# Optimization experiments

Hardware: AMD Instinct MI355X
Metric: run time of the kernel (lower is better)

Reference implementation:

```python
import jax, jax.numpy as jnp
import numpy as np

D_MODEL = 2048
D_FFN = 8192
TOP_K = 256


def setup_inputs() -> dict:
    key = jax.random.key(0)
    kx, kg, ku, kd = jax.random.split(key, 4)
    B, S = 4, 2048
    x = jax.random.normal(kx, (B, S, D_MODEL), dtype=jnp.float32)
    # kaiming_uniform_(a=sqrt(5)) on a 2D tensor -> U(-1/sqrt(fan_in), 1/sqrt(fan_in)),
    # where PyTorch's fan_in is size(1) of the parameter.
    bg = 1.0 / np.sqrt(D_FFN)
    w_gate = jax.random.uniform(kg, (D_MODEL, D_FFN), jnp.float32, -bg, bg)
    w_up = jax.random.uniform(ku, (D_MODEL, D_FFN), jnp.float32, -bg, bg)
    bd = 1.0 / np.sqrt(D_MODEL)
    w_down = jax.random.uniform(kd, (D_FFN, D_MODEL), jnp.float32, -bd, bd)
    return {"x": x, "w_gate": w_gate, "w_up": w_up, "w_down": w_down}


def reference(x, w_gate, w_up, w_down):
    orig_shape = x.shape
    xf = x.reshape(-1, x.shape[-1])          # [N, d_model]
    G = xf @ w_gate                           # [N, d_ffn]
    U = xf @ w_up                             # [N, d_ffn]
    _, idx = jax.lax.top_k(G, TOP_K)          # [N, k] int32 indices into d_ffn
    Gk = jnp.take_along_axis(G, idx, axis=-1)  # [N, k]
    Uk = jnp.take_along_axis(U, idx, axis=-1)  # [N, k]
    Z = jax.nn.silu(Gk) * Uk                   # fused sparse SiLU activation, [N, k]
    # Sparse-to-dense down projection: scatter the k active channels per token
    # back into d_ffn (top-k indices are unique per row, so .set is exact),
    # then a single dense matmul with w_down.
    N = G.shape[0]
    Zd = jnp.zeros((N, D_FFN), dtype=Z.dtype).at[jnp.arange(N)[:, None], idx].set(Z)
    out = Zd @ w_down                          # [N, d_model]
    return out.reshape(*orig_shape[:-1], w_down.shape[-1])
```

## Files before the change

kernel.cpp:

```cpp
#include <hip/hip_runtime.h>
#include <hip/hip_bf16.h>
#include <stdint.h>

#define D_MODEL 2048
#define D_FFN   8192
#define NTOK    8192
#define TOPK    256

typedef __bf16 bf16x8 __attribute__((ext_vector_type(8)));
typedef __bf16 bf16x4 __attribute__((ext_vector_type(4)));
typedef float  f32x4  __attribute__((ext_vector_type(4)));

__device__ inline void load_lds16(const void* g, void* l) {
    __builtin_amdgcn_global_load_lds((__attribute__((address_space(1))) void*)g,
                                     (__attribute__((address_space(3))) void*)l,
                                     16, 0, 0);
}

template<int NSEG, int SEGK, int LDC>
__global__ __attribute__((amdgpu_flat_work_group_size(512, 512),
                          amdgpu_waves_per_eu(2)))
void g256p(const __bf16* __restrict__ A0, const __bf16* __restrict__ A1,
           const __bf16* __restrict__ A2,
           const __bf16* __restrict__ B0, const __bf16* __restrict__ B1,
           const __bf16* __restrict__ B2,
           float* __restrict__ C)
{
    constexpr int NH  = NSEG * SEGK / 32;
    constexpr int NIT = NH / 4;

    __shared__ __align__(16) __bf16 sA[4][256][32];
    __shared__ __align__(16) __bf16 sB[4][256][32];

    const int tid  = threadIdx.x;
    const int lane = tid & 63;
    const int wid  = tid >> 6;
    const int mb   = blockIdx.y;
    const int nb   = blockIdx.x;

    const int wm = (wid >> 2) * 128;
    const int wn = (wid & 3) * 64;
    const int fr = lane & 15;
    const int q  = lane >> 4;

    const int swz8 = ((q ^ ((fr >> 1) & 3)) * 8);
    const int cl   = lane & 3;
    const int sr0  = wid * 32 + (lane >> 2);
    const int cg8a = (cl ^ ((sr0 >> 1) & 3)) * 8;

    f32x4 acc[8][4] = {};

    auto STAGE = [&](int op, int J) {
        const int s = J & 3;
        int seg = 0, kin = J * 32;
        if (NSEG > 1) { seg = (J * 32) / SEGK; kin = J * 32 - seg * SEGK; }
        const __bf16* base = op
            ? ((NSEG == 1 || seg == 0) ? B0 : (seg == 1 ? B1 : B2))
            : ((NSEG == 1 || seg == 0) ? A0 : (seg == 1 ? A1 : A2));
        const int rowbase = (op ? nb : mb) * 256;
        char* ldsb = (char*)(op ? &sB[s][0][0] : &sA[s][0][0]) + wid * 2048;
        #pragma unroll
        for (int p = 0; p < 2; ++p) {
            const int r = sr0 + p * 16;
            load_lds16(base + (size_t)(rowbase + r) * SEGK + kin + cg8a,
                       ldsb + p * 1024);
        }
    };

#define P_READ_B(s) { _Pragma("unroll") for (int ni = 0; ni < 4; ++ni) {       \
        const int r = wn + fr + ni * 16;                                       \
        bfr[ni] = *(const bf16x8*)&sB[s][r][swz8]; } }
#define P_READ_A(s, h) { _Pragma("unroll") for (int mi = 0; mi < 4; ++mi) {    \
        const int r = wm + (h) * 64 + fr + mi * 16;                            \
        af[mi] = *(const bf16x8*)&sA[s][r][swz8]; } }
#define P_MFMA(h) { __builtin_amdgcn_s_setprio(1);                             \
    _Pragma("unroll") for (int mi = 0; mi < 4; ++mi)                           \
    _Pragma("unroll") for (int ni = 0; ni < 4; ++ni)                           \
        acc[(h) * 4 + mi][ni] = __builtin_amdgcn_mfma_f32_16x16x32_bf16(       \
            af[mi], bfr[ni], acc[(h) * 4 + mi][ni], 0, 0, 0);                  \
    __builtin_amdgcn_s_setprio(0); }
#define P_STAGE2(Joff) { const int J = J0 + (Joff);                            \
        if (J >= 4 && J < NH) { STAGE(0, J); STAGE(1, J); } }
#define P_BAR  __builtin_amdgcn_s_barrier()
#define P_LGKM { asm volatile("s_waitcnt lgkmcnt(0)" ::: "memory");            \
                 __builtin_amdgcn_sched_barrier(0); }
#define SLOT_PHASE(sp, VM) {                                                   \
        P_READ_B(sp); P_READ_A(sp, 0);                                         \
        P_STAGE2(3 + (sp));                                                    \
        P_BAR; P_LGKM;                                                         \
        P_MFMA(0);                                                             \
        __builtin_amdgcn_sched_barrier(0);                                     \
        P_READ_A(sp, 1);                                                       \
        P_LGKM;                                                                \
        P_MFMA(1);                                                             \
        VM;                                                                    \
        P_BAR; }

    #pragma unroll
    for (int J = 0; J < 4; ++J) { STAGE(0, J); STAGE(1, J); }
    asm volatile("s_waitcnt vmcnt(0)" ::: "memory");
    P_BAR;

    for (int i = 0; i < NIT; ++i) {
        const int J0 = 4 * i;
        const bool last = (i == NIT - 1);
        bf16x8 af[4], bfr[4];

        SLOT_PHASE(0, );
        SLOT_PHASE(1,
            if (last) { asm volatile("s_waitcnt vmcnt(0)" ::: "memory"); }
            else      { asm volatile("s_waitcnt vmcnt(4)" ::: "memory"); });
        SLOT_PHASE(2, );
        SLOT_PHASE(3,
            if (last) { asm volatile("s_waitcnt vmcnt(0)" ::: "memory"); }
            else      { asm volatile("s_waitcnt vmcnt(4)" ::: "memory"); });
    }

#undef P_READ_B
#undef P_READ_A
#undef P_MFMA
#undef P_STAGE2
#undef P_BAR
#undef P_LGKM
#undef SLOT_PHASE

    const int orow = q * 4;
    #pragma unroll
    for (int ai = 0; ai < 8; ++ai) {
        const int rl = wm + (ai >> 2) * 64 + (ai & 3) * 16 + orow;
        #pragma unroll
        for (int ni = 0; ni < 4; ++ni)
            #pragma unroll
            for (int j = 0; j < 4; ++j) {
                const int r = mb * 256 + rl + j;
                const int c = nb * 256 + wn + ni * 16 + fr;
                C[(size_t)r * LDC + c] = acc[ai][ni][j];
            }
    }
}

template<int NSEG>
__global__ __launch_bounds__(256)
void gemm_bt(const __bf16* __restrict__ A0, const __bf16* __restrict__ A1,
             const __bf16* __restrict__ A2,
             const __bf16* __restrict__ B0, const __bf16* __restrict__ B1,
             const __bf16* __restrict__ B2,
             float* __restrict__ C, int segK, int ldc)
{
    __shared__ __align__(16) __bf16 sA[128][64];
    __shared__ __align__(16) __bf16 sB[128][64];

    const int tid  = threadIdx.x;
    const int lane = tid & 63;
    const int wid  = tid >> 6;
    const int mb   = blockIdx.y;
    const int nb   = blockIdx.x;

    f32x4 acc[4][4] = {};

    const int stR = wid * 8 + (lane >> 3);
    const int stC = (lane & 7) * 8;
    const int NKT = (NSEG * segK) / 64;

    for (int kt = 0; kt < NKT; ++kt) {
        const int kg  = kt * 64;
        const int seg = kg / segK;
        const int kin = kg - seg * segK;
        const __bf16* Aseg = (NSEG == 1 || seg == 0) ? A0 : (seg == 1 ? A1 : A2);
        const __bf16* Bseg = (NSEG == 1 || seg == 0) ? B0 : (seg == 1 ? B1 : B2);

        #pragma unroll
        for (int i = 0; i < 4; ++i) {
            const __bf16* gA = Aseg + (size_t)(mb * 128 + i * 32 + stR) * segK + (kin + stC);
            const __bf16* gB = Bseg + (size_t)(nb * 128 + i * 32 + stR) * segK + (kin + stC);
            load_lds16(gA, &sA[i * 32 + wid * 8][0]);
            load_lds16(gB, &sB[i * 32 + wid * 8][0]);
        }
        __syncthreads();

        const int wm = (wid >> 1) * 64;
        const int wn = (wid & 1) * 64;
        const int fr = lane & 15;
        const int fk = (lane >> 4) * 8;
        #pragma unroll
        for (int kk = 0; kk < 2; ++kk) {
            bf16x8 af[4], bfr[4];
            #pragma unroll
            for (int mi = 0; mi < 4; ++mi)
                af[mi] = *(const bf16x8*)&sA[wm + mi * 16 + fr][kk * 32 + fk];
            #pragma unroll
            for (int ni = 0; ni < 4; ++ni)
                bfr[ni] = *(const bf16x8*)&sB[wn + ni * 16 + fr][kk * 32 + fk];
            #pragma unroll
            for (int mi = 0; mi < 4; ++mi)
                #pragma unroll
                for (int ni = 0; ni < 4; ++ni)
                    acc[mi][ni] = __builtin_amdgcn_mfma_f32_16x16x32_bf16(
                        af[mi], bfr[ni], acc[mi][ni], 0, 0, 0);
        }
        __syncthreads();
    }

    const int wm = (wid >> 1) * 64;
    const int wn = (wid & 1) * 64;
    const int orow = (lane >> 4) * 4;
    const int ocol = lane & 15;
    #pragma unroll
    for (int mi = 0; mi < 4; ++mi)
        #pragma unroll
        for (int ni = 0; ni < 4; ++ni)
            #pragma unroll
            for (int j = 0; j < 4; ++j) {
                const int r = mb * 128 + wm + mi * 16 + orow + j;
                const int c = nb * 128 + wn + ni * 16 + ocol;
                C[(size_t)r * ldc + c] = acc[mi][ni][j];
            }
}

__global__ __launch_bounds__(256)
void split_convert(const float* __restrict__ in, __bf16* __restrict__ hi,
                   __bf16* __restrict__ lo, int n4)
{
    const int i = blockIdx.x * 256 + threadIdx.x;
    if (i >= n4) return;
    const float4 v = ((const float4*)in)[i];
    float f[4] = {v.x, v.y, v.z, v.w};
    bf16x4 h, l;
    #pragma unroll
    for (int j = 0; j < 4; ++j) {
        __bf16 hb = (__bf16)f[j];
        h[j] = hb;
        l[j] = (__bf16)(f[j] - (float)hb);
    }
    ((bf16x4*)hi)[i] = h;
    ((bf16x4*)lo)[i] = l;
}

template<bool SPLIT>
__global__ __launch_bounds__(256)
void transpose_bf16(const float* __restrict__ in, __bf16* __restrict__ outHi,
                    __bf16* __restrict__ outLo, int R, int C)
{
    __shared__ float tile[32][33];
    const int bx = blockIdx.x * 32;
    const int by = blockIdx.y * 32;
    const int tx = threadIdx.x & 31;
    const int ty = threadIdx.x >> 5;
    #pragma unroll
    for (int i = 0; i < 4; ++i)
        tile[ty + 8 * i][tx] = in[(size_t)(by + ty + 8 * i) * C + (bx + tx)];
    __syncthreads();
    #pragma unroll
    for (int i = 0; i < 4; ++i) {
        const float v = tile[tx][ty + 8 * i];
        const size_t o = (size_t)(bx + ty + 8 * i) * R + (by + tx);
        const __bf16 h = (__bf16)v;
        outHi[o] = h;
        if (SPLIT) outLo[o] = (__bf16)(v - (float)h);
    }
}

#define TK_EPS 3e-5f
#define TK_MAXA 64

__global__ __launch_bounds__(256)
void topk256(const float* __restrict__ G, const float* __restrict__ xblk,
             const float* __restrict__ wgate,
             int* __restrict__ idxOut, float* __restrict__ gkOut)
{
    const int row = blockIdx.x;
    const int t = threadIdx.x;
    const int lane = t & 63;
    const int wid  = t >> 6;

    __shared__ unsigned keys[D_FFN];
    __shared__ float    xr[D_MODEL];
    __shared__ unsigned hist[256];
    __shared__ unsigned scanb[256];
    __shared__ int      sIdx[TOPK];
    __shared__ float    sVal[TOPK];
    __shared__ int      ambIdx[TK_MAXA];
    __shared__ double   ambVal[TK_MAXA];
    __shared__ double   redW[4];
    __shared__ unsigned sh_bin, sh_above, sh_nc, sh_na, sh_fill;

    const float* g = G + (size_t)row * D_FFN;
    const float* xrow = xblk + (size_t)row * D_MODEL;
    for (int i = t; i < D_FFN; i += 256) {
        const unsigned u = __float_as_uint(g[i]);
        keys[i] = (u & 0x80000000u) ? ~u : (u | 0x80000000u);
    }
    for (int i = t; i < D_MODEL; i += 256) xr[i] = xrow[i];
    if (t == 0) { sh_nc = 0; sh_na = 0; sh_fill = 0; }
    __syncthreads();

    unsigned prefix = 0, pmask = 0;
    int remaining = TOPK;
    for (int shift = 24; shift >= 0; shift -= 8) {
        hist[t] = 0;
        __syncthreads();
        for (int i = t; i < D_FFN; i += 256) {
            const unsigned k = keys[i];
            if ((k & pmask) == prefix) atomicAdd(&hist[(k >> shift) & 255u], 1u);
        }
        __syncthreads();
        scanb[t] = hist[t];
        __syncthreads();
        for (int off = 1; off < 256; off <<= 1) {
            const unsigned add = (t + off < 256) ? scanb[t + off] : 0u;
            __syncthreads();
            scanb[t] += add;
            __syncthreads();
        }
        const unsigned above = (t == 255) ? 0u : scanb[t + 1];
        if (scanb[t] >= (unsigned)remaining && above < (unsigned)remaining) {
            sh_bin = (unsigned)t;
            sh_above = above;
        }
        __syncthreads();
        prefix |= sh_bin << shift;
        pmask  |= 0xFFu << shift;
        remaining -= (int)sh_above;
        __syncthreads();
    }
    const unsigned Tkey = prefix;
    const float vT = __uint_as_float((Tkey & 0x80000000u) ? (Tkey & 0x7FFFFFFFu) : ~Tkey);

    for (int i = t; i < D_FFN; i += 256) {
        const unsigned k = keys[i];
        const float f = __uint_as_float((k & 0x80000000u) ? (k & 0x7FFFFFFFu) : ~k);
        if (f > vT + TK_EPS) {
            const unsigned p = atomicAdd(&sh_nc, 1u);
            sIdx[p] = i;
            sVal[p] = f;
        } else if (f >= vT - TK_EPS) {
            const unsigned p = atomicAdd(&sh_na, 1u);
            if (p < TK_MAXA) ambIdx[p] = i;
        }
    }
    __syncthreads();
    const int nc = (int)sh_nc;
    const int na = min((int)sh_na, TK_MAXA);
    const int need = TOPK - nc;

    if (need >= na) {
        if (t < na) {
            const unsigned k = keys[ambIdx[t]];
            sIdx[nc + t] = ambIdx[t];
            sVal[nc + t] = __uint_as_float((k & 0x80000000u) ? (k & 0x7FFFFFFFu) : ~k);
        }
        __syncthreads();
    } else {
        for (int j = 0; j < na; ++j) {
            const int col = ambIdx[j];
            double p = 0.0;
            for (int k = t; k < D_MODEL; k += 256)
                p += (double)xr[k] * (double)wgate[(size_t)k * D_FFN + col];
            #pragma unroll
            for (int o = 32; o > 0; o >>= 1) p += __shfl_xor(p, o, 64);
            if (lane == 0) redW[wid] = p;
            __syncthreads();
            if (t == 0) ambVal[j] = (redW[0] + redW[1]) + (redW[2] + redW[3]);
            __syncthreads();
        }
        if (t < na) {
            const double v = ambVal[t];
            const int    c = ambIdx[t];
            int r = 0;
            for (int j = 0; j < na; ++j) {
                const double vj = ambVal[j];
                if (vj > v || (vj == v && ambIdx[j] < c)) r++;
            }
            if (r < need) {
                const unsigned p = atomicAdd(&sh_fill, 1u);
                sIdx[nc + p] = c;
                sVal[nc + p] = (float)v;
            }
        }
        __syncthreads();
    }

    idxOut[(size_t)row * TOPK + t] = sIdx[t];
    gkOut[(size_t)row * TOPK + t] = sVal[t];
}

__global__ __launch_bounds__(256)
void z_fused(const int* __restrict__ idx, const float* __restrict__ gk,
             const float* __restrict__ U, __bf16* __restrict__ Zd)
{
    const int r = blockIdx.x, t = threadIdx.x;
    const int p = r * TOPK + t;
    const int c = idx[p];
    const float g = gk[p];
    const float u = U[(size_t)r * D_FFN + c];
    const float s = g / (1.0f + __expf(-g));
    Zd[(size_t)r * D_FFN + c] = (__bf16)(s * u);
}

__global__ __launch_bounds__(256)
void zero_buf(float4* __restrict__ p, int n)
{
    int i = blockIdx.x * 256 + threadIdx.x;
    const int stride = gridDim.x * 256;
    for (; i < n; i += stride) p[i] = make_float4(0.f, 0.f, 0.f, 0.f);
}

extern "C" void kernel_launch(void* const* d_in, const int* in_sizes, int n_in,
                              void* d_out, int out_size, void* d_ws, size_t ws_size,
                              hipStream_t stream)
{
    const float* x  = (const float*)d_in[0];
    const float* wg = (const float*)d_in[1];
    const float* wu = (const float*)d_in[2];
    const float* wd = (const float*)d_in[3];
    float* out = (float*)d_out;

    const size_t SZ_XB = (size_t)NTOK * D_MODEL * 2;
    const size_t SZ_WB = (size_t)D_FFN * D_MODEL * 2;
    const size_t SZ_IK = (size_t)NTOK * TOPK * 4;
    char* ws = (char*)d_ws;
    size_t off = 0;
    auto alloc = [&](size_t bytes) -> char* {
        char* p = ws + off;
        off += (bytes + 255) & ~(size_t)255;
        return p;
    };
    __bf16* x_hi  = (__bf16*)alloc(SZ_XB);
    __bf16* x_lo  = (__bf16*)alloc(SZ_XB);
    __bf16* wT_a  = (__bf16*)alloc(SZ_WB);
    __bf16* wT_b  = (__bf16*)alloc(SZ_WB);
    int*    idx   = (int*)  alloc(SZ_IK);
    float*  gk    = (float*)alloc(SZ_IK);
    const size_t fixed = off;

    int RB = 2048;
    while (RB > 256 && fixed + (size_t)RB * D_FFN * 4 > ws_size) RB >>= 1;
    float* Eblk = (float*)alloc((size_t)RB * D_FFN * 4);
    __bf16* Zdb = x_lo;
    const int NRB = NTOK / RB;

    split_convert<<<(NTOK * D_MODEL / 4 + 255) / 256, 256, 0, stream>>>(
        x, x_hi, x_lo, NTOK * D_MODEL / 4);
    transpose_bf16<true><<<dim3(D_FFN / 32, D_MODEL / 32), 256, 0, stream>>>(
        wg, wT_a, wT_b, D_MODEL, D_FFN);

    for (int rb = 0; rb < NRB; ++rb) {
        const size_t aoff = (size_t)rb * RB * D_MODEL;
        g256p<3, D_MODEL, D_FFN><<<dim3(D_FFN / 256, RB / 256), 512, 0, stream>>>(
            x_hi + aoff, x_lo + aoff, x_hi + aoff,
            wT_a, wT_a, wT_b, Eblk);
        topk256<<<RB, 256, 0, stream>>>(
            Eblk, x + aoff, wg,
            idx + (size_t)rb * RB * TOPK, gk + (size_t)rb * RB * TOPK);
    }

    transpose_bf16<false><<<dim3(D_FFN / 32, D_MODEL / 32), 256, 0, stream>>>(
        wu, wT_a, nullptr, D_MODEL, D_FFN);
    transpose_bf16<false><<<dim3(D_MODEL / 32, D_FFN / 32), 256, 0, stream>>>(
        wd, wT_b, nullptr, D_FFN, D_MODEL);

    for (int rb = 0; rb < NRB; ++rb) {
        const size_t aoff = (size_t)rb * RB * D_MODEL;
        g256p<1, D_MODEL, D_FFN><<<dim3(D_FFN / 256, RB / 256), 512, 0, stream>>>(
            x_hi + aoff, nullptr, nullptr, wT_a, nullptr, nullptr, Eblk);
        zero_buf<<<2048, 256, 0, stream>>>((float4*)Zdb, RB * (D_FFN * 2 / 16));
        z_fused<<<RB, 256, 0, stream>>>(
            idx + (size_t)rb * RB * TOPK, gk + (size_t)rb * RB * TOPK, Eblk, Zdb);
        gemm_bt<1><<<dim3(D_MODEL / 128, RB / 128), 256, 0, stream>>>(
            Zdb, nullptr, nullptr, wT_b, nullptr, nullptr,
            out + (size_t)rb * RB * D_MODEL, D_FFN, D_MODEL);
    }
}
```

Before: 2.250 ms.

## Use single-bf16 gate GEMM with wider top-k ambiguity band and split-K down projection

The gate GEMM drops the three-pass hi/lo split-bf16 product and uses a single bf16 pass. To keep top-k selection exact, the ambiguity band around the threshold is widened, and candidates are first re-scored in parallel per wave using transposed hi+lo bf16 weights. The exact fp64 recompute from fp32 weights is kept only for candidates near the rank boundary. The down projection moves from the small 128-tile gemm_bt to the 256-tile pipelined kernel with split-K over blockIdx.z and atomic accumulation into an output zeroed beforehand. This trades fewer gate MFMA passes for more top-k refinement work and atomic output traffic, and it risks wrong selections when more than 96 near-threshold candidates appear in a row.

New measurement: 2.966 ms. 1.32x slower.

```diff
diff --git a/kernel.cpp b/kernel.cpp
--- a/kernel.cpp
+++ b/kernel.cpp
@@ -17,16 +17,13 @@
                                      16, 0, 0);
 }
 
-template<int NSEG, int SEGK, int LDC>
+template<int KEXT, int LDAB, int LDC, bool ATOMIC>
 __global__ __attribute__((amdgpu_flat_work_group_size(512, 512),
                           amdgpu_waves_per_eu(2)))
-void g256p(const __bf16* __restrict__ A0, const __bf16* __restrict__ A1,
-           const __bf16* __restrict__ A2,
-           const __bf16* __restrict__ B0, const __bf16* __restrict__ B1,
-           const __bf16* __restrict__ B2,
+void g256p(const __bf16* __restrict__ A, const __bf16* __restrict__ B,
            float* __restrict__ C)
 {
-    constexpr int NH  = NSEG * SEGK / 32;
+    constexpr int NH  = KEXT / 32;
     constexpr int NIT = NH / 4;
 
     __shared__ __align__(16) __bf16 sA[4][256][32];
@@ -38,6 +35,9 @@
     const int mb   = blockIdx.y;
     const int nb   = blockIdx.x;
 
+    A += (size_t)blockIdx.z * KEXT;
+    B += (size_t)blockIdx.z * KEXT;
+
     const int wm = (wid >> 2) * 128;
     const int wn = (wid & 3) * 64;
     const int fr = lane & 15;
@@ -52,17 +52,14 @@
 
     auto STAGE = [&](int op, int J) {
         const int s = J & 3;
-        int seg = 0, kin = J * 32;
-        if (NSEG > 1) { seg = (J * 32) / SEGK; kin = J * 32 - seg * SEGK; }
-        const __bf16* base = op
-            ? ((NSEG == 1 || seg == 0) ? B0 : (seg == 1 ? B1 : B2))
-            : ((NSEG == 1 || seg == 0) ? A0 : (seg == 1 ? A1 : A2));
+        const int kin = J * 32;
+        const __bf16* base = op ? B : A;
         const int rowbase = (op ? nb : mb) * 256;
         char* ldsb = (char*)(op ? &sB[s][0][0] : &sA[s][0][0]) + wid * 2048;
         #pragma unroll
         for (int p = 0; p < 2; ++p) {
             const int r = sr0 + p * 16;
-            load_lds16(base + (size_t)(rowbase + r) * SEGK + kin + cg8a,
+            load_lds16(base + (size_t)(rowbase + r) * LDAB + kin + cg8a,
                        ldsb + p * 1024);
         }
     };
@@ -134,106 +131,25 @@
             for (int j = 0; j < 4; ++j) {
                 const int r = mb * 256 + rl + j;
                 const int c = nb * 256 + wn + ni * 16 + fr;
-                C[(size_t)r * LDC + c] = acc[ai][ni][j];
+                if (ATOMIC)
+                    unsafeAtomicAdd(&C[(size_t)r * LDC + c], acc[ai][ni][j]);
+                else
+                    C[(size_t)r * LDC + c] = acc[ai][ni][j];
             }
     }
 }
 
-template<int NSEG>
 __global__ __launch_bounds__(256)
-void gemm_bt(const __bf16* __restrict__ A0, const __bf16* __restrict__ A1,
-             const __bf16* __restrict__ A2,
-             const __bf16* __restrict__ B0, const __bf16* __restrict__ B1,
-             const __bf16* __restrict__ B2,
-             float* __restrict__ C, int segK, int ldc)
-{
-    __shared__ __align__(16) __bf16 sA[128][64];
-    __shared__ __align__(16) __bf16 sB[128][64];
-
-    const int tid  = threadIdx.x;
-    const int lane = tid & 63;
-    const int wid  = tid >> 6;
-    const int mb   = blockIdx.y;
-    const int nb   = blockIdx.x;
-
-    f32x4 acc[4][4] = {};
-
-    const int stR = wid * 8 + (lane >> 3);
-    const int stC = (lane & 7) * 8;
-    const int NKT = (NSEG * segK) / 64;
-
-    for (int kt = 0; kt < NKT; ++kt) {
-        const int kg  = kt * 64;
-        const int seg = kg / segK;
-        const int kin = kg - seg * segK;
-        const __bf16* Aseg = (NSEG == 1 || seg == 0) ? A0 : (seg == 1 ? A1 : A2);
-        const __bf16* Bseg = (NSEG == 1 || seg == 0) ? B0 : (seg == 1 ? B1 : B2);
-
-        #pragma unroll
-        for (int i = 0; i < 4; ++i) {
-            const __bf16* gA = Aseg + (size_t)(mb * 128 + i * 32 + stR) * segK + (kin + stC);
-            const __bf16* gB = Bseg + (size_t)(nb * 128 + i * 32 + stR) * segK + (kin + stC);
-            load_lds16(gA, &sA[i * 32 + wid * 8][0]);
-            load_lds16(gB, &sB[i * 32 + wid * 8][0]);
-        }
-        __syncthreads();
-
-        const int wm = (wid >> 1) * 64;
-        const int wn = (wid & 1) * 64;
-        const int fr = lane & 15;
-        const int fk = (lane >> 4) * 8;
-        #pragma unroll
-        for (int kk = 0; kk < 2; ++kk) {
-            bf16x8 af[4], bfr[4];
-            #pragma unroll
-            for (int mi = 0; mi < 4; ++mi)
-                af[mi] = *(const bf16x8*)&sA[wm + mi * 16 + fr][kk * 32 + fk];
-            #pragma unroll
-            for (int ni = 0; ni < 4; ++ni)
-                bfr[ni] = *(const bf16x8*)&sB[wn + ni * 16 + fr][kk * 32 + fk];
-            #pragma unroll
-            for (int mi = 0; mi < 4; ++mi)
-                #pragma unroll
-                for (int ni = 0; ni < 4; ++ni)
-                    acc[mi][ni] = __builtin_amdgcn_mfma_f32_16x16x32_bf16(
-                        af[mi], bfr[ni], acc[mi][ni], 0, 0, 0);
-        }
-        __syncthreads();
-    }
-
-    const int wm = (wid >> 1) * 64;
-    const int wn = (wid & 1) * 64;
-    const int orow = (lane >> 4) * 4;
-    const int ocol = lane & 15;
-    #pragma unroll
-    for (int mi = 0; mi < 4; ++mi)
-        #pragma unroll
-        for (int ni = 0; ni < 4; ++ni)
-            #pragma unroll
-            for (int j = 0; j < 4; ++j) {
-                const int r = mb * 128 + wm + mi * 16 + orow + j;
-                const int c = nb * 128 + wn + ni * 16 + ocol;
-                C[(size_t)r * ldc + c] = acc[mi][ni][j];
-            }
-}
-
-__global__ __launch_bounds__(256)
-void split_convert(const float* __restrict__ in, __bf16* __restrict__ hi,
-                   __bf16* __restrict__ lo, int n4)
+void convert_hi(const float* __restrict__ in, __bf16* __restrict__ hi, int n4)
 {
     const int i = blockIdx.x * 256 + threadIdx.x;
     if (i >= n4) return;
     const float4 v = ((const float4*)in)[i];
     float f[4] = {v.x, v.y, v.z, v.w};
-    bf16x4 h, l;
+    bf16x4 h;
     #pragma unroll
-    for (int j = 0; j < 4; ++j) {
-        __bf16 hb = (__bf16)f[j];
-        h[j] = hb;
-        l[j] = (__bf16)(f[j] - (float)hb);
-    }
+    for (int j = 0; j < 4; ++j) h[j] = (__bf16)f[j];
     ((bf16x4*)hi)[i] = h;
-    ((bf16x4*)lo)[i] = l;
 }
 
 template<bool SPLIT>
@@ -260,11 +176,13 @@
     }
 }
 
-#define TK_EPS 3e-5f
-#define TK_MAXA 64
+#define TK_CEPS 8e-3f
+#define TK_REPS 2e-5
+#define TK_MAXA 96
 
 __global__ __launch_bounds__(256)
 void topk256(const float* __restrict__ G, const float* __restrict__ xblk,
+             const __bf16* __restrict__ wgTh, const __bf16* __restrict__ wgTl,
              const float* __restrict__ wgate,
              int* __restrict__ idxOut, float* __restrict__ gkOut)
 {
@@ -282,6 +200,7 @@
     __shared__ int      ambIdx[TK_MAXA];
     __shared__ double   ambVal[TK_MAXA];
     __shared__ double   redW[4];
+    __shared__ double   sh_vR;
     __shared__ unsigned sh_bin, sh_above, sh_nc, sh_na, sh_fill;
 
     const float* g = G + (size_t)row * D_FFN;
@@ -329,11 +248,11 @@
     for (int i = t; i < D_FFN; i += 256) {
         const unsigned k = keys[i];
         const float f = __uint_as_float((k & 0x80000000u) ? (k & 0x7FFFFFFFu) : ~k);
-        if (f > vT + TK_EPS) {
+        if (f > vT + TK_CEPS) {
             const unsigned p = atomicAdd(&sh_nc, 1u);
             sIdx[p] = i;
             sVal[p] = f;
-        } else if (f >= vT - TK_EPS) {
+        } else if (f >= vT - TK_CEPS) {
             const unsigned p = atomicAdd(&sh_na, 1u);
             if (p < TK_MAXA) ambIdx[p] = i;
         }
@@ -351,17 +270,43 @@
         }
         __syncthreads();
     } else {
-        for (int j = 0; j < na; ++j) {
+        for (int j = wid; j < na; j += 4) {
             const int col = ambIdx[j];
+            const __bf16* ch = wgTh + (size_t)col * D_MODEL;
+            const __bf16* cl2 = wgTl + (size_t)col * D_MODEL;
             double p = 0.0;
-            for (int k = t; k < D_MODEL; k += 256)
-                p += (double)xr[k] * (double)wgate[(size_t)k * D_FFN + col];
+            for (int k = lane; k < D_MODEL; k += 64)
+                p += (double)xr[k] * ((double)(float)ch[k] + (double)(float)cl2[k]);
             #pragma unroll
             for (int o = 32; o > 0; o >>= 1) p += __shfl_xor(p, o, 64);
-            if (lane == 0) redW[wid] = p;
-            __syncthreads();
-            if (t == 0) ambVal[j] = (redW[0] + redW[1]) + (redW[2] + redW[3]);
-            __syncthreads();
+            if (lane == 0) ambVal[j] = p;
+        }
+        __syncthreads();
+        if (t < na) {
+            const double v = ambVal[t];
+            const int    c = ambIdx[t];
+            int r = 0;
+            for (int j = 0; j < na; ++j) {
+                const double vj = ambVal[j];
+                if (vj > v || (vj == v && ambIdx[j] < c)) r++;
+            }
+            if (r == need - 1) sh_vR = v;
+        }
+        __syncthreads();
+        const double vR = sh_vR;
+        for (int j = 0; j < na; ++j) {
+            if (fabs(ambVal[j] - vR) <= TK_REPS) {
+                const int col = ambIdx[j];
+                double p = 0.0;
+                for (int k = t; k < D_MODEL; k += 256)
+                    p += (double)xr[k] * (double)wgate[(size_t)k * D_FFN + col];
+                #pragma unroll
+                for (int o = 32; o > 0; o >>= 1) p += __shfl_xor(p, o, 64);
+                if (lane == 0) redW[wid] = p;
+                __syncthreads();
+                if (t == 0) ambVal[j] = (redW[0] + redW[1]) + (redW[2] + redW[3]);
+                __syncthreads();
+            }
         }
         if (t < na) {
             const double v = ambVal[t];
@@ -426,7 +371,7 @@
         return p;
     };
     __bf16* x_hi  = (__bf16*)alloc(SZ_XB);
-    __bf16* x_lo  = (__bf16*)alloc(SZ_XB);
+    __bf16* zbuf  = (__bf16*)alloc(SZ_XB);
     __bf16* wT_a  = (__bf16*)alloc(SZ_WB);
     __bf16* wT_b  = (__bf16*)alloc(SZ_WB);
     int*    idx   = (int*)  alloc(SZ_IK);
@@ -436,21 +381,20 @@
     int RB = 2048;
     while (RB > 256 && fixed + (size_t)RB * D_FFN * 4 > ws_size) RB >>= 1;
     float* Eblk = (float*)alloc((size_t)RB * D_FFN * 4);
-    __bf16* Zdb = x_lo;
     const int NRB = NTOK / RB;
 
-    split_convert<<<(NTOK * D_MODEL / 4 + 255) / 256, 256, 0, stream>>>(
-        x, x_hi, x_lo, NTOK * D_MODEL / 4);
+    convert_hi<<<(NTOK * D_MODEL / 4 + 255) / 256, 256, 0, stream>>>(
+        x, x_hi, NTOK * D_MODEL / 4);
     transpose_bf16<true><<<dim3(D_FFN / 32, D_MODEL / 32), 256, 0, stream>>>(
         wg, wT_a, wT_b, D_MODEL, D_FFN);
 
     for (int rb = 0; rb < NRB; ++rb) {
         const size_t aoff = (size_t)rb * RB * D_MODEL;
-        g256p<3, D_MODEL, D_FFN><<<dim3(D_FFN / 256, RB / 256), 512, 0, stream>>>(
-            x_hi + aoff, x_lo + aoff, x_hi + aoff,
-            wT_a, wT_a, wT_b, Eblk);
+        g256p<D_MODEL, D_MODEL, D_FFN, false>
+            <<<dim3(D_FFN / 256, RB / 256), 512, 0, stream>>>(
+                x_hi + aoff, wT_a, Eblk);
         topk256<<<RB, 256, 0, stream>>>(
-            Eblk, x + aoff, wg,
+            Eblk, x + aoff, wT_a, wT_b, wg,
             idx + (size_t)rb * RB * TOPK, gk + (size_t)rb * RB * TOPK);
     }
 
@@ -459,15 +403,19 @@
     transpose_bf16<false><<<dim3(D_MODEL / 32, D_FFN / 32), 256, 0, stream>>>(
         wd, wT_b, nullptr, D_FFN, D_MODEL);
 
+    zero_buf<<<4096, 256, 0, stream>>>(
+        (float4*)out, (int)((size_t)NTOK * D_MODEL * 4 / 16));
+
     for (int rb = 0; rb < NRB; ++rb) {
         const size_t aoff = (size_t)rb * RB * D_MODEL;
-        g256p<1, D_MODEL, D_FFN><<<dim3(D_FFN / 256, RB / 256), 512, 0, stream>>>(
-            x_hi + aoff, nullptr, nullptr, wT_a, nullptr, nullptr, Eblk);
-        zero_buf<<<2048, 256, 0, stream>>>((float4*)Zdb, RB * (D_FFN * 2 / 16));
+        g256p<D_MODEL, D_MODEL, D_FFN, false>
+            <<<dim3(D_FFN / 256, RB / 256), 512, 0, stream>>>(
+                x_hi + aoff, wT_a, Eblk);
+        zero_buf<<<2048, 256, 0, stream>>>((float4*)zbuf, RB * (D_FFN * 2 / 16));
         z_fused<<<RB, 256, 0, stream>>>(
-            idx + (size_t)rb * RB * TOPK, gk + (size_t)rb * RB * TOPK, Eblk, Zdb);
-        gemm_bt<1><<<dim3(D_MODEL / 128, RB / 128), 256, 0, stream>>>(
-            Zdb, nullptr, nullptr, wT_b, nullptr, nullptr,
-            out + (size_t)rb * RB * D_MODEL, D_FFN, D_MODEL);
-    }
-}
+            idx + (size_t)rb * RB * TOPK, gk + (size_t)rb * RB * TOPK, Eblk, zbuf);
+        g256p<D_MODEL, D_FFN, D_MODEL, true>
+            <<<dim3(D_MODEL / 256, RB / 256, D_FFN / D_MODEL), 512, 0, stream>>>(
+                zbuf, wT_b, out + aoff);
+    }
+}
```

## Run down projection through pipelined 256-tile GEMM with split-K atomic accumulation

Applied to the files above, without the earlier changes.

Generalizes the pipelined 256x256 GEMM kernel with separate leading dimensions, a blockIdx.z K offset and an optional atomic-add epilogue. The down projection, which previously used the simple 128-tile gemm_bt kernel, now runs on it with a 4-way split-K to get enough blocks for the small 2048-wide output. The output is zeroed first. This adds float atomic traffic on the output and makes the summation order nondeterministic.

Result: faster. 2.064 ms (-8.3%).

```diff
diff --git a/kernel.cpp b/kernel.cpp
--- a/kernel.cpp
+++ b/kernel.cpp
@@ -17,7 +17,7 @@
                                      16, 0, 0);
 }
 
-template<int NSEG, int SEGK, int LDC>
+template<int NSEG, int SEGK, int LDA, int LDB, int LDC, bool ATOMIC>
 __global__ __attribute__((amdgpu_flat_work_group_size(512, 512),
                           amdgpu_waves_per_eu(2)))
 void g256p(const __bf16* __restrict__ A0, const __bf16* __restrict__ A1,
@@ -26,8 +26,9 @@
            const __bf16* __restrict__ B2,
            float* __restrict__ C)
 {
-    constexpr int NH  = NSEG * SEGK / 32;
-    constexpr int NIT = NH / 4;
+    constexpr int KEXT = NSEG * SEGK;
+    constexpr int NH   = KEXT / 32;
+    constexpr int NIT  = NH / 4;
 
     __shared__ __align__(16) __bf16 sA[4][256][32];
     __shared__ __align__(16) __bf16 sB[4][256][32];
@@ -37,6 +38,9 @@
     const int wid  = tid >> 6;
     const int mb   = blockIdx.y;
     const int nb   = blockIdx.x;
+
+    const size_t zoff = (size_t)blockIdx.z * KEXT;
+    A0 += zoff; B0 += zoff;
 
     const int wm = (wid >> 2) * 128;
     const int wn = (wid & 3) * 64;
@@ -58,11 +62,12 @@
             ? ((NSEG == 1 || seg == 0) ? B0 : (seg == 1 ? B1 : B2))
             : ((NSEG == 1 || seg == 0) ? A0 : (seg == 1 ? A1 : A2));
         const int rowbase = (op ? nb : mb) * 256;
+        const int ld = op ? LDB : LDA;
         char* ldsb = (char*)(op ? &sB[s][0][0] : &sA[s][0][0]) + wid * 2048;
         #pragma unroll
         for (int p = 0; p < 2; ++p) {
             const int r = sr0 + p * 16;
-            load_lds16(base + (size_t)(rowbase + r) * SEGK + kin + cg8a,
+            load_lds16(base + (size_t)(rowbase + r) * ld + kin + cg8a,
                        ldsb + p * 1024);
         }
     };
@@ -134,87 +139,12 @@
             for (int j = 0; j < 4; ++j) {
                 const int r = mb * 256 + rl + j;
                 const int c = nb * 256 + wn + ni * 16 + fr;
-                C[(size_t)r * LDC + c] = acc[ai][ni][j];
+                if (ATOMIC)
+                    unsafeAtomicAdd(&C[(size_t)r * LDC + c], acc[ai][ni][j]);
+                else
+                    C[(size_t)r * LDC + c] = acc[ai][ni][j];
             }
     }
-}
-
-template<int NSEG>
-__global__ __launch_bounds__(256)
-void gemm_bt(const __bf16* __restrict__ A0, const __bf16* __restrict__ A1,
-             const __bf16* __restrict__ A2,
-             const __bf16* __restrict__ B0, const __bf16* __restrict__ B1,
-             const __bf16* __restrict__ B2,
-             float* __restrict__ C, int segK, int ldc)
-{
-    __shared__ __align__(16) __bf16 sA[128][64];
-    __shared__ __align__(16) __bf16 sB[128][64];
-
-    const int tid  = threadIdx.x;
-    const int lane = tid & 63;
-    const int wid  = tid >> 6;
-    const int mb   = blockIdx.y;
-    const int nb   = blockIdx.x;
-
-    f32x4 acc[4][4] = {};
-
-    const int stR = wid * 8 + (lane >> 3);
-    const int stC = (lane & 7) * 8;
-    const int NKT = (NSEG * segK) / 64;
-
-    for (int kt = 0; kt < NKT; ++kt) {
-        const int kg  = kt * 64;
-        const int seg = kg / segK;
-        const int kin = kg - seg * segK;
-        const __bf16* Aseg = (NSEG == 1 || seg == 0) ? A0 : (seg == 1 ? A1 : A2);
-        const __bf16* Bseg = (NSEG == 1 || seg == 0) ? B0 : (seg == 1 ? B1 : B2);
-
-        #pragma unroll
-        for (int i = 0; i < 4; ++i) {
-            const __bf16* gA = Aseg + (size_t)(mb * 128 + i * 32 + stR) * segK + (kin + stC);
-            const __bf16* gB = Bseg + (size_t)(nb * 128 + i * 32 + stR) * segK + (kin + stC);
-            load_lds16(gA, &sA[i * 32 + wid * 8][0]);
-            load_lds16(gB, &sB[i * 32 + wid * 8][0]);
-        }
-        __syncthreads();
-
-        const int wm = (wid >> 1) * 64;
-        const int wn = (wid & 1) * 64;
-        const int fr = lane & 15;
-        const int fk = (lane >> 4) * 8;
-        #pragma unroll
-        for (int kk = 0; kk < 2; ++kk) {
-            bf16x8 af[4], bfr[4];
-            #pragma unroll
-            for (int mi = 0; mi < 4; ++mi)
-                af[mi] = *(const bf16x8*)&sA[wm + mi * 16 + fr][kk * 32 + fk];
-            #pragma unroll
-            for (int ni = 0; ni < 4; ++ni)
-                bfr[ni] = *(const bf16x8*)&sB[wn + ni * 16 + fr][kk * 32 + fk];
-            #pragma unroll
-            for (int mi = 0; mi < 4; ++mi)
-                #pragma unroll
-                for (int ni = 0; ni < 4; ++ni)
-                    acc[mi][ni] = __builtin_amdgcn_mfma_f32_16x16x32_bf16(
-                        af[mi], bfr[ni], acc[mi][ni], 0, 0, 0);
-        }
-        __syncthreads();
-    }
-
-    const int wm = (wid >> 1) * 64;
-    const int wn = (wid & 1) * 64;
-    const int orow = (lane >> 4) * 4;
-    const int ocol = lane & 15;
-    #pragma unroll
-    for (int mi = 0; mi < 4; ++mi)
-        #pragma unroll
-        for (int ni = 0; ni < 4; ++ni)
-            #pragma unroll
-            for (int j = 0; j < 4; ++j) {
-                const int r = mb * 128 + wm + mi * 16 + orow + j;
-                const int c = nb * 128 + wn + ni * 16 + ocol;
-                C[(size_t)r * ldc + c] = acc[mi][ni][j];
-            }
 }
 
 __global__ __launch_bounds__(256)
@@ -446,9 +376,10 @@
 
     for (int rb = 0; rb < NRB; ++rb) {
         const size_t aoff = (size_t)rb * RB * D_MODEL;
-        g256p<3, D_MODEL, D_FFN><<<dim3(D_FFN / 256, RB / 256), 512, 0, stream>>>(
-            x_hi + aoff, x_lo + aoff, x_hi + aoff,
-            wT_a, wT_a, wT_b, Eblk);
+        g256p<3, D_MODEL, D_MODEL, D_MODEL, D_FFN, false>
+            <<<dim3(D_FFN / 256, RB / 256, 1), 512, 0, stream>>>(
+                x_hi + aoff, x_lo + aoff, x_hi + aoff,
+                wT_a, wT_a, wT_b, Eblk);
         topk256<<<RB, 256, 0, stream>>>(
             Eblk, x + aoff, wg,
             idx + (size_t)rb * RB * TOPK, gk + (size_t)rb * RB * TOPK);
@@ -459,15 +390,19 @@
     transpose_bf16<false><<<dim3(D_MODEL / 32, D_FFN / 32), 256, 0, stream>>>(
         wd, wT_b, nullptr, D_FFN, D_MODEL);
 
+    zero_buf<<<4096, 256, 0, stream>>>(
+        (float4*)out, (int)((size_t)NTOK * D_MODEL * 4 / 16));
+
     for (int rb = 0; rb < NRB; ++rb) {
         const size_t aoff = (size_t)rb * RB * D_MODEL;
-        g256p<1, D_MODEL, D_FFN><<<dim3(D_FFN / 256, RB / 256), 512, 0, stream>>>(
-            x_hi + aoff, nullptr, nullptr, wT_a, nullptr, nullptr, Eblk);
+        g256p<1, D_MODEL, D_MODEL, D_MODEL, D_FFN, false>
+            <<<dim3(D_FFN / 256, RB / 256, 1), 512, 0, stream>>>(
+                x_hi + aoff, nullptr, nullptr, wT_a, nullptr, nullptr, Eblk);
         zero_buf<<<2048, 256, 0, stream>>>((float4*)Zdb, RB * (D_FFN * 2 / 16));
         z_fused<<<RB, 256, 0, stream>>>(
             idx + (size_t)rb * RB * TOPK, gk + (size_t)rb * RB * TOPK, Eblk, Zdb);
-        gemm_bt<1><<<dim3(D_MODEL / 128, RB / 128), 256, 0, stream>>>(
-            Zdb, nullptr, nullptr, wT_b, nullptr, nullptr,
-            out + (size_t)rb * RB * D_MODEL, D_FFN, D_MODEL);
-    }
-}
+        g256p<1, D_MODEL, D_FFN, D_FFN, D_MODEL, true>
+            <<<dim3(D_MODEL / 256, RB / 256, D_FFN / D_MODEL), 512, 0, stream>>>(
+                Zdb, nullptr, nullptr, wT_b, nullptr, nullptr, out + aoff);
+    }
+}
```
